# Optimization experiments

Hardware: AMD Instinct MI355X
Metric: run time of the kernel (lower is better)

The kernel has to match this reference:

```python
import jax, jax.numpy as jnp
import numpy as np

BANDWIDTH = 1.0
EPS = 1e-20


def setup_inputs() -> dict:
    key = jax.random.key(0)
    k1, k2, k3 = jax.random.split(key, 3)
    test_X = jax.random.normal(k1, (8192, 64), dtype=jnp.float32)
    train_X = jax.random.normal(k2, (16384, 64), dtype=jnp.float32)
    sample_weight = jax.random.uniform(k3, (16384,), dtype=jnp.float32)
    return {"test_X": test_X, "train_X": train_X, "sample_weight": sample_weight}


def reference(test_X, train_X, sample_weight):
    # test_X: [m, d], train_X: [n, d], sample_weight: [n]
    d = train_X.shape[1]
    h = jnp.float32(BANDWIDTH)
    # weights are normalized; with weights, n is treated as 1 => log(n) = 0
    w = sample_weight / jnp.sum(sample_weight)
    Z = 0.5 * d * jnp.log(2.0 * jnp.float32(np.pi)) + d * jnp.log(h)
    # squared L2 distances via expansion (avoids [m, n, d] intermediate)
    t2 = jnp.sum(test_X * test_X, axis=-1)  # [m]
    r2 = jnp.sum(train_X * train_X, axis=-1)  # [n]
    cross = test_X @ train_X.T  # [m, n]
    sq = (t2[:, None] + r2[None, :] - 2.0 * cross) / (h * h)  # [m, n]
    val = -0.5 * sq - Z  # [m, n]
    # weighted, numerically-stable log-sum-exp over train dim
    m_max = jnp.max(val, axis=-1, keepdims=True)  # [m, 1]
    s = jnp.sum(jnp.exp(val - m_max) * w[None, :], axis=-1)  # [m]
    return m_max[:, 0] + jnp.log(s + EPS)
```

## Files before the change

### kernel.cpp

```cpp
#include <hip/hip_runtime.h>
#include <hip/hip_bf16.h>
#include <math.h>

#define M 8192
#define N 16384
#define D 64
#define ZC 58.81206612509905f
#define B0 24.0f
#define LOG2E 1.4426950408889634f
#define HL2E 0.7213475204444817f
#define LN2 0.6931471805599453f

#define PCH 16
#define NCHK (N / PCH)

typedef short v8bf __attribute__((ext_vector_type(8)));
typedef float v16f __attribute__((ext_vector_type(16)));

#define B_AU2  0
#define B_LW2  32768
#define B_PART 98304
#define B_TB   622592
#define B_TR   1671168

__global__ __launch_bounds__(256) void gk_prep(const float* __restrict__ testX,
                                               const float* __restrict__ trainX,
                                               const float* __restrict__ sw,
                                               __hip_bfloat16* __restrict__ tb,
                                               __hip_bfloat16* __restrict__ rb,
                                               float* __restrict__ au2,
                                               float* __restrict__ lw2) {
    const int tid = threadIdx.x;
    const int e = tid & 7;
    if (blockIdx.x < M / 32) {
        const int row = blockIdx.x * 32 + (tid >> 3);
        const float4* p = reinterpret_cast<const float4*>(testX + (size_t)row * D + e * 8);
        float4 v0 = p[0], v1 = p[1];
        float t2 = v0.x * v0.x + v0.y * v0.y + v0.z * v0.z + v0.w * v0.w
                 + v1.x * v1.x + v1.y * v1.y + v1.z * v1.z + v1.w * v1.w;
        t2 += __shfl_xor(t2, 1, 64);
        t2 += __shfl_xor(t2, 2, 64);
        t2 += __shfl_xor(t2, 4, 64);
        if (e == 0) au2[row] = -HL2E * t2;
        union { __hip_bfloat16 h[8]; uint4 u; } cv;
        cv.h[0] = __float2bfloat16(v0.x * LOG2E);
        cv.h[1] = __float2bfloat16(v0.y * LOG2E);
        cv.h[2] = __float2bfloat16(v0.z * LOG2E);
        cv.h[3] = __float2bfloat16(v0.w * LOG2E);
        cv.h[4] = __float2bfloat16(v1.x * LOG2E);
        cv.h[5] = __float2bfloat16(v1.y * LOG2E);
        cv.h[6] = __float2bfloat16(v1.z * LOG2E);
        cv.h[7] = __float2bfloat16(v1.w * LOG2E);
        *reinterpret_cast<uint4*>(tb + (size_t)row * D + e * 8) = cv.u;
    } else {
        const int row = (blockIdx.x - M / 32) * 32 + (tid >> 3);
        const float4* p = reinterpret_cast<const float4*>(trainX + (size_t)row * D + e * 8);
        float4 v0 = p[0], v1 = p[1];
        float r2 = v0.x * v0.x + v0.y * v0.y + v0.z * v0.z + v0.w * v0.w
                 + v1.x * v1.x + v1.y * v1.y + v1.z * v1.z + v1.w * v1.w;
        r2 += __shfl_xor(r2, 1, 64);
        r2 += __shfl_xor(r2, 2, 64);
        r2 += __shfl_xor(r2, 4, 64);
        if (e == 0) lw2[row] = __builtin_amdgcn_logf(sw[row]) - HL2E * r2 + B0;
        union { __hip_bfloat16 h[8]; uint4 u; } cv;
        cv.h[0] = __float2bfloat16(v0.x);
        cv.h[1] = __float2bfloat16(v0.y);
        cv.h[2] = __float2bfloat16(v0.z);
        cv.h[3] = __float2bfloat16(v0.w);
        cv.h[4] = __float2bfloat16(v1.x);
        cv.h[5] = __float2bfloat16(v1.y);
        cv.h[6] = __float2bfloat16(v1.z);
        cv.h[7] = __float2bfloat16(v1.w);
        *reinterpret_cast<uint4*>(rb + (size_t)row * D + e * 8) = cv.u;
    }
}

__device__ __forceinline__ void dma16(const void* g, void* l) {
    __builtin_amdgcn_global_load_lds(
        (const __attribute__((address_space(1))) unsigned int*)g,
        (__attribute__((address_space(3))) unsigned int*)l, 16, 0, 0);
}

__device__ __forceinline__ void dma_tile(const __hip_bfloat16* tr, int nt,
                                         char* Bsb, int w, int lane) {
#pragma unroll
    for (int i = 0; i < 2; ++i) {
        const int g = w * 2 + i;
        const __hip_bfloat16* gp =
            tr + (size_t)(nt + g * 8 + (lane & 7)) * D + (lane >> 3) * 8;
        dma16(gp, Bsb + g * 1024);
    }
}

__device__ __forceinline__ void compute_tile(const char* Bs, float lwa, float lwb,
                                             const v8bf af[4], float srun[16],
                                             int c, int h) {
#pragma unroll
    for (int s = 0; s < 2; ++s) {
        const float lwv = s ? lwb : lwa;
        v16f acc;
#pragma unroll
        for (int r = 0; r < 16; ++r) acc[r] = lwv;
#pragma unroll
        for (int t = 0; t < 4; ++t) {
            const v8bf bf = *reinterpret_cast<const v8bf*>(
                Bs + (s * 4 + (c >> 3)) * 1024 + (2 * t + h) * 128 + (c & 7) * 16);
            acc = __builtin_amdgcn_mfma_f32_32x32x16_bf16(af[t], bf, acc, 0, 0, 0);
        }
#pragma unroll
        for (int r = 0; r < 16; ++r)
            srun[r] += __builtin_amdgcn_exp2f(acc[r]);
    }
}

__global__ __launch_bounds__(256, 4) void gk_main(const __hip_bfloat16* __restrict__ ta,
                                                  const __hip_bfloat16* __restrict__ tr,
                                                  const float* __restrict__ lw2,
                                                  float* __restrict__ part) {
    __shared__ __align__(16) char smem[16896];
    const int tid = threadIdx.x;
    const int w = tid >> 6;
    const int lane = tid & 63;
    const int c = lane & 31;
    const int h = lane >> 5;

    const int bid = blockIdx.x;
    const int xcd = bid & 7;
    const int j = bid >> 3;
    const int chunk = xcd * 2 + (j & 1);
    const int m0 = (j >> 1) * 128;
    const int n0 = chunk * NCHK;

    char* const Bs0 = smem;
    char* const Bs1 = smem + 8192;

    dma_tile(tr, n0, Bs0, w, lane);
    float lwa0 = lw2[n0 + c], lwb0 = lw2[n0 + 32 + c];

    const __hip_bfloat16* arow = ta + (size_t)(m0 + w * 32 + c) * D;
    v8bf af[4];
#pragma unroll
    for (int t = 0; t < 4; ++t)
        af[t] = *reinterpret_cast<const v8bf*>(arow + (2 * t + h) * 8);

    float srun[16];
#pragma unroll
    for (int r = 0; r < 16; ++r) srun[r] = 0.f;

    __syncthreads();

#pragma unroll
    for (int s8 = 0; s8 < 8; ++s8) {
        const int t0 = s8 * 2;
        dma_tile(tr, n0 + (t0 + 1) * 64, Bs1, w, lane);
        const float lwa1 = lw2[n0 + (t0 + 1) * 64 + c];
        const float lwb1 = lw2[n0 + (t0 + 1) * 64 + 32 + c];
        compute_tile(Bs0, lwa0, lwb0, af, srun, c, h);
        __syncthreads();
        if (t0 + 2 < 16) {
            dma_tile(tr, n0 + (t0 + 2) * 64, Bs0, w, lane);
            lwa0 = lw2[n0 + (t0 + 2) * 64 + c];
            lwb0 = lw2[n0 + (t0 + 2) * 64 + 32 + c];
        }
        compute_tile(Bs1, lwa1, lwb1, af, srun, c, h);
        __syncthreads();
    }

    float* red = reinterpret_cast<float*>(smem);
#pragma unroll
    for (int r = 0; r < 16; ++r) {
        int rowl = (r & 3) + 8 * (r >> 2) + 4 * h;
        red[(w * 32 + rowl) * 33 + c] = srun[r];
    }
    __syncthreads();
    if (tid < 128) {
        float G = 0.f;
#pragma unroll
        for (int c2 = 0; c2 < 32; ++c2) G += red[tid * 33 + c2];
        part[(size_t)chunk * M + m0 + tid] = G;
    }
}

__global__ __launch_bounds__(256) void gk_merge(const float* __restrict__ part,
                                                const float* __restrict__ au2,
                                                const float* __restrict__ sw,
                                                float* __restrict__ out) {
    __shared__ float red[256];
    const int tid = threadIdx.x;
    float s = 0.f;
    const float4* p4 = reinterpret_cast<const float4*>(sw);
    for (int i = tid; i < N / 4; i += 256) {
        float4 v = p4[i];
        s += v.x + v.y + v.z + v.w;
    }
    red[tid] = s;
    __syncthreads();
    for (int off = 128; off > 0; off >>= 1) {
        if (tid < off) red[tid] += red[tid + off];
        __syncthreads();
    }
    const float W = red[0];

    const int r = blockIdx.x * 256 + tid;
    float G = 0.f;
#pragma unroll
    for (int p = 0; p < PCH; ++p) G += part[(size_t)p * M + r];
    out[r] = LN2 * (au2[r] + __builtin_amdgcn_logf(fmaxf(G, 1e-30f)) - B0
                   - __builtin_amdgcn_logf(W)) - ZC;
}

extern "C" void kernel_launch(void* const* d_in, const int* in_sizes, int n_in,
                              void* d_out, int out_size, void* d_ws, size_t ws_size,
                              hipStream_t stream) {
    const float* testX  = (const float*)d_in[0];
    const float* trainX = (const float*)d_in[1];
    const float* sw     = (const float*)d_in[2];
    float* out = (float*)d_out;
    char* wsb = (char*)d_ws;

    float* au2  = (float*)(wsb + B_AU2);
    float* lw2  = (float*)(wsb + B_LW2);
    float* part = (float*)(wsb + B_PART);
    __hip_bfloat16* tb = (__hip_bfloat16*)(wsb + B_TB);
    __hip_bfloat16* rb = (__hip_bfloat16*)(wsb + B_TR);

    gk_prep<<<M / 32 + N / 32, 256, 0, stream>>>(testX, trainX, sw, tb, rb, au2, lw2);
    gk_main<<<(M / 128) * PCH, 256, 0, stream>>>(tb, rb, lw2, part);
    gk_merge<<<M / 256, 256, 0, stream>>>(part, au2, sw, out);
}
```

Baseline: 93.15 us.

## Triple-buffer train tiles with explicit vmcnt waits and one barrier per tile

Replaces the double-buffered LDS pipeline, which needed two __syncthreads per tile pair, with a three-stage ring buffer. Loads are issued two tiles ahead, and each tile uses a partial s_waitcnt vmcnt plus a single s_barrier, so DMA latency overlaps more MFMA/exp work and there is less barrier stalling. LDS grows from about 16.5KB to 24KB per block, which may limit occupancy. Correctness depends on the hand-counted vmcnt values, since the lw2 scalar loads also count toward vmcnt.

After: 94.14 us. No clear change (+1.1%).

```diff
diff --git a/kernel.cpp b/kernel.cpp
--- a/kernel.cpp
+++ b/kernel.cpp
@@ -117,7 +117,7 @@
                                                   const __hip_bfloat16* __restrict__ tr,
                                                   const float* __restrict__ lw2,
                                                   float* __restrict__ part) {
-    __shared__ __align__(16) char smem[16896];
+    __shared__ __align__(16) char smem[24576];
     const int tid = threadIdx.x;
     const int w = tid >> 6;
     const int lane = tid & 63;
@@ -131,11 +131,12 @@
     const int m0 = (j >> 1) * 128;
     const int n0 = chunk * NCHK;
 
-    char* const Bs0 = smem;
-    char* const Bs1 = smem + 8192;
-
-    dma_tile(tr, n0, Bs0, w, lane);
-    float lwa0 = lw2[n0 + c], lwb0 = lw2[n0 + 32 + c];
+    char* const Bs[3] = { smem, smem + 8192, smem + 16384 };
+
+    float lwa[3], lwb[3];
+
+    dma_tile(tr, n0, Bs[0], w, lane);
+    lwa[0] = lw2[n0 + c]; lwb[0] = lw2[n0 + 32 + c];
 
     const __hip_bfloat16* arow = ta + (size_t)(m0 + w * 32 + c) * D;
     v8bf af[4];
@@ -143,29 +144,30 @@
     for (int t = 0; t < 4; ++t)
         af[t] = *reinterpret_cast<const v8bf*>(arow + (2 * t + h) * 8);
 
+    dma_tile(tr, n0 + 64, Bs[1], w, lane);
+    lwa[1] = lw2[n0 + 64 + c]; lwb[1] = lw2[n0 + 96 + c];
+
     float srun[16];
 #pragma unroll
     for (int r = 0; r < 16; ++r) srun[r] = 0.f;
 
+#pragma unroll
+    for (int t = 0; t < 16; ++t) {
+        if (t < 15) {
+            asm volatile("s_waitcnt vmcnt(4)" ::: "memory");
+        } else {
+            asm volatile("s_waitcnt vmcnt(0)" ::: "memory");
+        }
+        __builtin_amdgcn_s_barrier();
+        if (t + 2 < 16) {
+            dma_tile(tr, n0 + (t + 2) * 64, Bs[(t + 2) % 3], w, lane);
+            lwa[(t + 2) % 3] = lw2[n0 + (t + 2) * 64 + c];
+            lwb[(t + 2) % 3] = lw2[n0 + (t + 2) * 64 + 32 + c];
+        }
+        compute_tile(Bs[t % 3], lwa[t % 3], lwb[t % 3], af, srun, c, h);
+    }
+
     __syncthreads();
-
-#pragma unroll
-    for (int s8 = 0; s8 < 8; ++s8) {
-        const int t0 = s8 * 2;
-        dma_tile(tr, n0 + (t0 + 1) * 64, Bs1, w, lane);
-        const float lwa1 = lw2[n0 + (t0 + 1) * 64 + c];
-        const float lwb1 = lw2[n0 + (t0 + 1) * 64 + 32 + c];
-        compute_tile(Bs0, lwa0, lwb0, af, srun, c, h);
-        __syncthreads();
-        if (t0 + 2 < 16) {
-            dma_tile(tr, n0 + (t0 + 2) * 64, Bs0, w, lane);
-            lwa0 = lw2[n0 + (t0 + 2) * 64 + c];
-            lwb0 = lw2[n0 + (t0 + 2) * 64 + 32 + c];
-        }
-        compute_tile(Bs1, lwa1, lwb1, af, srun, c, h);
-        __syncthreads();
-    }
-
     float* red = reinterpret_cast<float*>(smem);
 #pragma unroll
     for (int r = 0; r < 16; ++r) {
```
